# Performance work log

Measured on AMD Instinct MI355X. Metric: run time of the kernel, lower is better.

The kernel has to match this reference:

```python
import jax, jax.numpy as jnp
import numpy as np

POOLED_H = 7
POOLED_W = 7
SPATIAL_SCALE = 0.0625
IMG = 896  # image size -> 56x56 feature map at stride 16


def setup_inputs() -> dict:
    key = jax.random.key(0)
    kf, kb, kx1, kx2, ky1, ky2 = jax.random.split(key, 6)
    B, C, H, W = 4, 256, 56, 56
    N = 256
    features = jax.random.normal(kf, (B, C, H, W), dtype=jnp.float32)
    b = jax.random.randint(kb, (N,), 0, B)
    x1 = jax.random.randint(kx1, (N,), 0, IMG)
    y1 = jax.random.randint(ky1, (N,), 0, IMG)
    x2 = jnp.clip(x1 + jax.random.randint(kx2, (N,), 0, IMG), None, IMG - 1)
    y2 = jnp.clip(y1 + jax.random.randint(ky2, (N,), 0, IMG), None, IMG - 1)
    rois = jnp.stack([b, x1, y1, x2, y2], axis=1).astype(jnp.float32)
    return {"features": features, "rois": rois}


def reference(features, rois):
    # Faithful RoIPool (pool_type='MAX'):
    #   rois[:,1:] *= spatial_scale; rois = rois.long()  (truncation; coords >= 0 so == floor)
    #   crop features[b, :, y1:y2+1, x1:x2+1] and adaptive_max_pool2d to (7,7).
    B, C, H, W = features.shape
    N = rois.shape[0]
    r = rois.at[:, 1:].multiply(SPATIAL_SCALE).astype(jnp.int32)
    b, x1, y1, x2, y2 = r[:, 0], r[:, 1], r[:, 2], r[:, 3], r[:, 4]
    roi_h = y2 - y1 + 1  # crop uses y2+1 inclusive end
    roi_w = x2 - x1 + 1
    # adaptive pool bins for length L, out size o: start=floor(i*L/o), end=ceil((i+1)*L/o)
    # max bin width is bounded by ceil(H/o)+1, a static quantity -> jit friendly.
    MBH = -(-H // POOLED_H) + 1
    MBW = -(-W // POOLED_W) + 1
    ph = jnp.arange(POOLED_H)
    pw = jnp.arange(POOLED_W)

    hs = y1[:, None] + (ph[None, :] * roi_h[:, None]) // POOLED_H              # [N,7]
    he = y1[:, None] + ((ph[None, :] + 1) * roi_h[:, None] + POOLED_H - 1) // POOLED_H
    kh = jnp.arange(MBH)
    h_idx = jnp.clip(hs[:, :, None] + kh, 0, H - 1)                            # [N,7,MBH]
    h_valid = kh[None, None, :] < (he - hs)[:, :, None]                        # [N,7,MBH]

    ws = x1[:, None] + (pw[None, :] * roi_w[:, None]) // POOLED_W              # [N,7]
    we = x1[:, None] + ((pw[None, :] + 1) * roi_w[:, None] + POOLED_W - 1) // POOLED_W
    kw = jnp.arange(MBW)
    w_idx = jnp.clip(ws[:, :, None] + kw, 0, W - 1)                            # [N,7,MBW]
    w_valid = kw[None, None, :] < (we - ws)[:, :, None]                        # [N,7,MBW]

    fb = features[b]  # [N,C,H,W] per-ROI feature maps
    # max over the rectangle is separable: max over rows, then over cols.
    gh = jax.vmap(lambda f, hi: f[:, hi, :])(fb, h_idx)                        # [N,C,7,MBH,W]
    gh = jnp.where(h_valid[:, None, :, :, None], gh, -jnp.inf).max(axis=3)     # [N,C,7,W]
    gw = jax.vmap(lambda f, wi: f[:, :, wi])(gh, w_idx)                        # [N,C,7,7,MBW]
    out = jnp.where(w_valid[:, None, None, :, :], gw, -jnp.inf).max(axis=-1)   # [N,C,7,7]
    return out
```

## Files before the change

### kernel.cpp

```cpp
#include <hip/hip_runtime.h>
#include <math.h>

#define POOLED 7
#define SCALE 0.0625f
#define C_ 256
#define H_ 56
#define W_ 56
#define S_ (H_ * W_)
#define NCELL 49

typedef _Float16 f16x4 __attribute__((ext_vector_type(4)));
typedef _Float16 f16x8 __attribute__((ext_vector_type(8)));

__device__ __forceinline__ f16x8 max8h(f16x8 a, f16x8 b) {
    f16x8 r;
    #pragma unroll
    for (int i = 0; i < 8; ++i) r[i] = a[i] > b[i] ? a[i] : b[i];
    return r;
}

__global__ __launch_bounds__(1024) void nhwc_kernel(
    const float* __restrict__ src, _Float16* __restrict__ dst)
{
    __shared__ float tile[64][65];
    int b = blockIdx.z;
    int sbase = blockIdx.x * 64;
    int cbase = blockIdx.y * 64;
    int tid = threadIdx.x;

    const float* s0 = src + (size_t)b * C_ * S_;
    _Float16* d0 = dst + (size_t)b * S_ * C_;

    {
        int si = tid & 15;
        int c  = tid >> 4;
        float4 v = *(const float4*)(s0 + (size_t)(cbase + c) * S_ + sbase + 4 * si);
        tile[4 * si + 0][c] = v.x;
        tile[4 * si + 1][c] = v.y;
        tile[4 * si + 2][c] = v.z;
        tile[4 * si + 3][c] = v.w;
    }
    __syncthreads();
    {
        int cj = tid & 15;
        int s  = tid >> 4;
        f16x4 pk;
        pk[0] = (_Float16)tile[s][4 * cj + 0];
        pk[1] = (_Float16)tile[s][4 * cj + 1];
        pk[2] = (_Float16)tile[s][4 * cj + 2];
        pk[3] = (_Float16)tile[s][4 * cj + 3];
        *(f16x4*)(d0 + (size_t)(sbase + s) * C_ + cbase + 4 * cj) = pk;
    }
}

__global__ __launch_bounds__(256) void pool_fused_kernel(
    const _Float16* __restrict__ t, const float* __restrict__ rois,
    float* __restrict__ out)
{
    __shared__ float stage[4][257];
    int b0   = blockIdx.x;
    int swz  = (b0 & 7) * 416 + (b0 >> 3);
    int n    = swz / 13;
    int cg   = swz % 13;
    int wv   = threadIdx.x >> 6;
    int lane = threadIdx.x & 63;
    int cell = cg * 4 + wv;

    const float* r = rois + n * 5;
    int b  = (int)r[0];
    int x1 = (int)(r[1] * SCALE);
    int y1 = (int)(r[2] * SCALE);
    int x2 = (int)(r[3] * SCALE);
    int y2 = (int)(r[4] * SCALE);
    int rh = y2 - y1 + 1;
    int rw = x2 - x1 + 1;

    if (cell < NCELL) {
        int ph = cell / POOLED;
        int pw = cell % POOLED;
        int hs = y1 + (ph * rh) / POOLED;
        int he = y1 + ((ph + 1) * rh + POOLED - 1) / POOLED;
        int ws = x1 + (pw * rw) / POOLED;
        int we = x1 + ((pw + 1) * rw + POOLED - 1) / POOLED;
        int nh = he - hs;
        int nw = we - ws;

        int pos = lane >> 5;
        int c8  = lane & 31;

        const f16x8* base = (const f16x8*)(t + (size_t)b * S_ * C_) + c8
                            + (size_t)(hs * W_ + ws) * 32;

        const _Float16 NEGV = (_Float16)(-65504.0f);
        f16x8 a0 = {NEGV, NEGV, NEGV, NEGV, NEGV, NEGV, NEGV, NEGV};
        f16x8 a1 = a0, a2 = a0, a3 = a0;

        for (int h = 0; h < nh; h += 2) {
            int h1 = (h + 1 < nh) ? h + 1 : h;
            const f16x8* hp0 = base + (size_t)h  * (W_ * 32);
            const f16x8* hp1 = base + (size_t)h1 * (W_ * 32);
            for (int w = 0; w < nw; w += 4) {
                int o0 = w + pos;     if (o0 >= nw) o0 = nw - 1;
                int o1 = w + 2 + pos; if (o1 >= nw) o1 = nw - 1;
                a0 = max8h(a0, hp0[(size_t)o0 * 32]);
                a1 = max8h(a1, hp0[(size_t)o1 * 32]);
                a2 = max8h(a2, hp1[(size_t)o0 * 32]);
                a3 = max8h(a3, hp1[(size_t)o1 * 32]);
            }
        }
        f16x8 m = max8h(max8h(a0, a1), max8h(a2, a3));

        union { f16x8 h8; unsigned int u[4]; } A, B;
        A.h8 = m;
        #pragma unroll
        for (int k = 0; k < 4; ++k) B.u[k] = __shfl_xor(A.u[k], 32, 64);
        m = max8h(A.h8, B.h8);

        if (lane < 32) {
            #pragma unroll
            for (int j = 0; j < 8; ++j)
                stage[wv][8 * c8 + j] = (float)m[j];
        }
    }
    __syncthreads();

    float* dst = out + (size_t)n * C_ * NCELL + cg * 4;
    if (cg < 12) {
        #pragma unroll
        for (int k = 0; k < 4; ++k) {
            int f = threadIdx.x + 256 * k;
            int c = f >> 2, j = f & 3;
            dst[(size_t)c * NCELL + j] = stage[j][c];
        }
    } else {
        dst[(size_t)threadIdx.x * NCELL] = stage[0][threadIdx.x];
    }
}

__global__ __launch_bounds__(256) void roipool_direct_kernel(
    const float* __restrict__ feat, const float* __restrict__ rois,
    float* __restrict__ out, int total)
{
    int idx = blockIdx.x * blockDim.x + threadIdx.x;
    if (idx >= total) return;
    int pw = idx % POOLED;
    int ph = (idx / POOLED) % POOLED;
    int c  = (idx / (POOLED * POOLED)) % C_;
    int n  = idx / (POOLED * POOLED * C_);
    const float* r = rois + n * 5;
    int b  = (int)r[0];
    int x1 = (int)(r[1] * SCALE);
    int y1 = (int)(r[2] * SCALE);
    int x2 = (int)(r[3] * SCALE);
    int y2 = (int)(r[4] * SCALE);
    int rh = y2 - y1 + 1;
    int rw = x2 - x1 + 1;
    int hs = y1 + (ph * rh) / POOLED;
    int he = y1 + ((ph + 1) * rh + POOLED - 1) / POOLED;
    int ws = x1 + (pw * rw) / POOLED;
    int we = x1 + ((pw + 1) * rw + POOLED - 1) / POOLED;
    const float* plane = feat + ((size_t)b * C_ + c) * (size_t)S_;
    float m = -INFINITY;
    for (int h = hs; h < he; ++h) {
        const float* row = plane + h * W_;
        for (int w = ws; w < we; ++w) m = fmaxf(m, row[w]);
    }
    out[idx] = m;
}

extern "C" void kernel_launch(void* const* d_in, const int* in_sizes, int n_in,
                              void* d_out, int out_size, void* d_ws, size_t ws_size,
                              hipStream_t stream) {
    const float* feat = (const float*)d_in[0];
    const float* rois = (const float*)d_in[1];
    float* out = (float*)d_out;

    int N = in_sizes[1] / 5;
    size_t featBytes = (size_t)4 * S_ * C_ * sizeof(_Float16);

    if (ws_size >= featBytes && N == 256) {
        _Float16* t = (_Float16*)d_ws;

        dim3 tgrid(S_ / 64, C_ / 64, 4);
        nhwc_kernel<<<tgrid, 1024, 0, stream>>>(feat, t);

        pool_fused_kernel<<<3328, 256, 0, stream>>>(t, rois, out);
    } else {
        int total = N * C_ * POOLED * POOLED;
        roipool_direct_kernel<<<(total + 255) / 256, 256, 0, stream>>>(feat, rois, out, total);
    }
}
```

Before: 30.69 us.

## Fuse NHWC transpose and ROI pooling into one cooperative persistent kernel

Replaces the two launches (fp32 NCHW to fp16 NHWC transpose, then ROI max pooling) with a single cooperative kernel. Blocks first loop over transpose tiles, meet at a grid-wide barrier, then loop over pooling units. This removes one launch and the gap between kernels. In exchange it adds a grid sync, a host-side occupancy query on every call, and persistent grid-stride loops that may balance work less evenly, and it falls back to the old path if the cooperative launch fails.

Result: slower. 93.49 us (+204.6%).

```diff
diff --git a/kernel.cpp b/kernel.cpp
--- a/kernel.cpp
+++ b/kernel.cpp
@@ -1,5 +1,8 @@
 #include <hip/hip_runtime.h>
+#include <hip/hip_cooperative_groups.h>
 #include <math.h>
+
+namespace cgx = cooperative_groups;
 
 #define POOLED 7
 #define SCALE 0.0625f
@@ -19,31 +22,34 @@
     return r;
 }
 
-__global__ __launch_bounds__(1024) void nhwc_kernel(
-    const float* __restrict__ src, _Float16* __restrict__ dst)
-{
-    __shared__ float tile[64][65];
-    int b = blockIdx.z;
-    int sbase = blockIdx.x * 64;
-    int cbase = blockIdx.y * 64;
-    int tid = threadIdx.x;
-
-    const float* s0 = src + (size_t)b * C_ * S_;
-    _Float16* d0 = dst + (size_t)b * S_ * C_;
-
-    {
-        int si = tid & 15;
-        int c  = tid >> 4;
-        float4 v = *(const float4*)(s0 + (size_t)(cbase + c) * S_ + sbase + 4 * si);
-        tile[4 * si + 0][c] = v.x;
-        tile[4 * si + 1][c] = v.y;
-        tile[4 * si + 2][c] = v.z;
-        tile[4 * si + 3][c] = v.w;
-    }
-    __syncthreads();
-    {
-        int cj = tid & 15;
-        int s  = tid >> 4;
+__device__ __forceinline__ void nhwc_tile_body(
+    const float* __restrict__ feat, _Float16* __restrict__ t,
+    int v, int tid, float (*tile)[65])
+{
+    int b     = v / 196;
+    int rem   = v % 196;
+    int cbase = (rem / 49) * 64;
+    int sbase = (rem % 49) * 64;
+    const float* s0 = feat + (size_t)b * C_ * S_;
+    _Float16*    d0 = t    + (size_t)b * S_ * C_;
+
+    int si = tid & 15;
+    int ci = tid >> 4;
+    #pragma unroll
+    for (int p = 0; p < 4; ++p) {
+        int c = ci + 16 * p;
+        float4 vv = *(const float4*)(s0 + (size_t)(cbase + c) * S_ + sbase + 4 * si);
+        tile[4 * si + 0][c] = vv.x;
+        tile[4 * si + 1][c] = vv.y;
+        tile[4 * si + 2][c] = vv.z;
+        tile[4 * si + 3][c] = vv.w;
+    }
+    __syncthreads();
+    int cj = tid & 15;
+    int sj = tid >> 4;
+    #pragma unroll
+    for (int p = 0; p < 4; ++p) {
+        int s = sj + 16 * p;
         f16x4 pk;
         pk[0] = (_Float16)tile[s][4 * cj + 0];
         pk[1] = (_Float16)tile[s][4 * cj + 1];
@@ -51,19 +57,18 @@
         pk[3] = (_Float16)tile[s][4 * cj + 3];
         *(f16x4*)(d0 + (size_t)(sbase + s) * C_ + cbase + 4 * cj) = pk;
     }
-}
-
-__global__ __launch_bounds__(256) void pool_fused_kernel(
+    __syncthreads();
+}
+
+__device__ __forceinline__ void pool_unit_body(
     const _Float16* __restrict__ t, const float* __restrict__ rois,
-    float* __restrict__ out)
-{
-    __shared__ float stage[4][257];
-    int b0   = blockIdx.x;
-    int swz  = (b0 & 7) * 416 + (b0 >> 3);
+    float* __restrict__ out, int u, int tid, float (*stage)[257])
+{
+    int swz  = (u & 7) * 416 + (u >> 3);
     int n    = swz / 13;
     int cg   = swz % 13;
-    int wv   = threadIdx.x >> 6;
-    int lane = threadIdx.x & 63;
+    int wv   = tid >> 6;
+    int lane = tid & 63;
     int cell = cg * 4 + wv;
 
     const float* r = rois + n * 5;
@@ -110,10 +115,10 @@
         }
         f16x8 m = max8h(max8h(a0, a1), max8h(a2, a3));
 
-        union { f16x8 h8; unsigned int u[4]; } A, B;
+        union { f16x8 h8; unsigned int uu[4]; } A, B;
         A.h8 = m;
         #pragma unroll
-        for (int k = 0; k < 4; ++k) B.u[k] = __shfl_xor(A.u[k], 32, 64);
+        for (int k = 0; k < 4; ++k) B.uu[k] = __shfl_xor(A.uu[k], 32, 64);
         m = max8h(A.h8, B.h8);
 
         if (lane < 32) {
@@ -128,13 +133,75 @@
     if (cg < 12) {
         #pragma unroll
         for (int k = 0; k < 4; ++k) {
-            int f = threadIdx.x + 256 * k;
+            int f = tid + 256 * k;
             int c = f >> 2, j = f & 3;
             dst[(size_t)c * NCELL + j] = stage[j][c];
         }
     } else {
-        dst[(size_t)threadIdx.x * NCELL] = stage[0][threadIdx.x];
-    }
+        dst[(size_t)tid * NCELL] = stage[0][tid];
+    }
+    __syncthreads();
+}
+
+__global__ __launch_bounds__(256) void fused_kernel(
+    const float* __restrict__ feat, const float* __restrict__ rois,
+    _Float16* __restrict__ t, float* __restrict__ out, int nblocks)
+{
+    __shared__ union {
+        float tile[64][65];
+        float stage[4][257];
+    } sh;
+    int tid = threadIdx.x;
+
+    for (int v = blockIdx.x; v < 784; v += nblocks)
+        nhwc_tile_body(feat, t, v, tid, sh.tile);
+
+    cgx::this_grid().sync();
+
+    for (int u = blockIdx.x; u < 3328; u += nblocks)
+        pool_unit_body(t, rois, out, u, tid, sh.stage);
+}
+
+__global__ __launch_bounds__(1024) void nhwc_kernel(
+    const float* __restrict__ src, _Float16* __restrict__ dst)
+{
+    __shared__ float tile[64][65];
+    int b = blockIdx.z;
+    int sbase = blockIdx.x * 64;
+    int cbase = blockIdx.y * 64;
+    int tid = threadIdx.x;
+
+    const float* s0 = src + (size_t)b * C_ * S_;
+    _Float16* d0 = dst + (size_t)b * S_ * C_;
+
+    {
+        int si = tid & 15;
+        int c  = tid >> 4;
+        float4 v = *(const float4*)(s0 + (size_t)(cbase + c) * S_ + sbase + 4 * si);
+        tile[4 * si + 0][c] = v.x;
+        tile[4 * si + 1][c] = v.y;
+        tile[4 * si + 2][c] = v.z;
+        tile[4 * si + 3][c] = v.w;
+    }
+    __syncthreads();
+    {
+        int cj = tid & 15;
+        int s  = tid >> 4;
+        f16x4 pk;
+        pk[0] = (_Float16)tile[s][4 * cj + 0];
+        pk[1] = (_Float16)tile[s][4 * cj + 1];
+        pk[2] = (_Float16)tile[s][4 * cj + 2];
+        pk[3] = (_Float16)tile[s][4 * cj + 3];
+        *(f16x4*)(d0 + (size_t)(sbase + s) * C_ + cbase + 4 * cj) = pk;
+    }
+}
+
+__global__ __launch_bounds__(256) void pool_fused_kernel(
+    const _Float16* __restrict__ t, const float* __restrict__ rois,
+    float* __restrict__ out)
+{
+    __shared__ float stage[4][257];
+    pool_unit_body(t, rois, out, blockIdx.x, threadIdx.x, stage);
 }
 
 __global__ __launch_bounds__(256) void roipool_direct_kernel(
@@ -181,9 +248,21 @@
     if (ws_size >= featBytes && N == 256) {
         _Float16* t = (_Float16*)d_ws;
 
+        int maxB = 0;
+        hipError_t qe = hipOccupancyMaxActiveBlocksPerMultiprocessor(
+            &maxB, (const void*)fused_kernel, 256, 0);
+
+        if (qe == hipSuccess && maxB > 0) {
+            int grid = maxB * 256;
+            if (grid > 3328) grid = 3328;
+            void* args[] = { (void*)&feat, (void*)&rois, (void*)&t, (void*)&out, (void*)&grid };
+            hipError_t le = hipLaunchCooperativeKernel(
+                (const void*)fused_kernel, dim3(grid), dim3(256), args, 0, stream);
+            if (le == hipSuccess) return;
+        }
+
         dim3 tgrid(S_ / 64, C_ / 64, 4);
         nhwc_kernel<<<tgrid, 1024, 0, stream>>>(feat, t);
-
         pool_fused_kernel<<<3328, 256, 0, stream>>>(t, rois, out);
     } else {
         int total = N * C_ * POOLED * POOLED;
```
